# Kernel optimization log

Hardware: AMD Instinct MI355X
Metric: run time of the kernel (lower is better)

## Reference

```python
import jax, jax.numpy as jnp
import numpy as np

SHAPES = ((496, 432), (248, 216), (124, 108))
NS = (40000, 20000, 8000)
T = 32
B = 4
EPS = 1e-3


def _bn(x, g, b, m, v):
    return (x - m) * (g / jnp.sqrt(v + EPS)) + b


def _vfe_scale(voxels, num_pts, w1, p1, w2, p2):
    # voxels: (N, T, 4); num_pts: (N,)
    Tp = voxels.shape[1]
    n = num_pts.astype(voxels.dtype)[:, None, None]
    m3 = voxels[:, :, :3].sum(axis=1, keepdims=True) / n
    m2 = voxels[:, :, :2].sum(axis=1, keepdims=True) / n
    feat = jnp.concatenate([voxels[:, :, :4], voxels[:, :, :3] - m3, voxels[:, :, :2] - m2], axis=-1)  # (N,T,9)
    mask = (jnp.arange(Tp)[None, :] < num_pts[:, None]).astype(voxels.dtype)[:, :, None]
    x = feat
    for w, (g, b_, rm, rv) in ((w1, p1), (w2, p2)):
        h = jax.nn.relu(_bn(jnp.einsum('ntc,cd->ntd', x, w), g, b_, rm, rv))  # (N,T,64)
        gmax = h.max(axis=1, keepdims=True)  # global max includes padded rows, as in torch source
        x = jnp.concatenate([h, jnp.broadcast_to(gmax, h.shape)], axis=-1) * mask  # (N,T,128)
    return x.max(axis=1)[:, :64]  # (N,64)


def _scatter_bev(vf, coords, h, w, batch_size):
    b = coords[:, 0]
    y = jnp.clip(coords[:, 2], 0, h - 1)
    x = jnp.clip(coords[:, 3], 0, w - 1)
    grid = jnp.zeros((batch_size, vf.shape[1], h, w), vf.dtype)
    return grid.at[b, :, y, x].set(vf)


def _fusion(x, w, g, b, m, v):
    y = jax.lax.conv_general_dilated(x, w, (1, 1), ((1, 1), (1, 1)),
                                     dimension_numbers=('NCHW', 'OIHW', 'NCHW'))
    y = _bn(y, g[None, :, None, None], b[None, :, None, None], m[None, :, None, None], v[None, :, None, None])
    return jax.nn.relu(y)


def setup_inputs() -> dict:
    key = jax.random.key(0)
    ks = jax.random.split(key, 32)
    inp = {}
    for s in range(3):
        h, w = SHAPES[s]
        inp[f'voxels_{s}'] = jax.random.normal(ks[s], (NS[s], T, 4), dtype=jnp.float32)
        inp[f'num_pts_{s}'] = jax.random.randint(ks[3 + s], (NS[s],), 1, T + 1, dtype=jnp.int32)
        b = jax.random.randint(ks[6 + s], (NS[s],), 0, B, dtype=jnp.int32)
        z = jnp.zeros((NS[s],), jnp.int32)
        y = jax.random.randint(ks[9 + s], (NS[s],), 0, h, dtype=jnp.int32)
        x = jax.random.randint(ks[12 + s], (NS[s],), 0, w, dtype=jnp.int32)
        inp[f'coords_{s}'] = jnp.stack([b, z, y, x], axis=1)
    # VFE params (stacked across the 3 scales; identical shapes per scale)
    inp['w1'] = jax.random.normal(ks[15], (3, 9, 64), dtype=jnp.float32) * 0.1
    inp['g1'] = jnp.ones((3, 64), jnp.float32) + 0.1 * jax.random.normal(ks[16], (3, 64))
    inp['b1'] = 0.05 * jax.random.normal(ks[17], (3, 64))
    inp['rm1'] = 0.05 * jax.random.normal(ks[18], (3, 64))
    inp['rv1'] = 0.5 + jnp.abs(jax.random.normal(ks[19], (3, 64)))
    inp['w2'] = jax.random.normal(ks[20], (3, 128, 64), dtype=jnp.float32) * 0.05
    inp['g2'] = jnp.ones((3, 64), jnp.float32) + 0.1 * jax.random.normal(ks[21], (3, 64))
    inp['b2'] = 0.05 * jax.random.normal(ks[22], (3, 64))
    inp['rm2'] = 0.05 * jax.random.normal(ks[23], (3, 64))
    inp['rv2'] = 0.5 + jnp.abs(jax.random.normal(ks[24], (3, 64)))
    # Fusion convs (2): Conv2d(128,64,3) + BN
    inp['fw'] = jax.random.normal(ks[25], (2, 64, 128, 3, 3), dtype=jnp.float32) * 0.03
    inp['fg'] = jnp.ones((2, 64), jnp.float32) + 0.1 * jax.random.normal(ks[26], (2, 64))
    inp['fb'] = 0.05 * jax.random.normal(ks[27], (2, 64))
    inp['fm'] = 0.05 * jax.random.normal(ks[28], (2, 64))
    inp['fv'] = 0.5 + jnp.abs(jax.random.normal(ks[29], (2, 64)))
    inp['batch_size'] = B
    return inp


def reference(voxels_0, voxels_1, voxels_2,
              w1, g1, b1, rm1, rv1, w2, g2, b2, rm2, rv2,
              fw, fg, fb, fm, fv,
              num_pts_0, num_pts_1, num_pts_2,
              coords_0, coords_1, coords_2, batch_size):
    voxels = (voxels_0, voxels_1, voxels_2)
    num_pts = (num_pts_0, num_pts_1, num_pts_2)
    coords = (coords_0, coords_1, coords_2)
    sf = []
    for s in range(3):
        vf = _vfe_scale(voxels[s], num_pts[s],
                        w1[s], (g1[s], b1[s], rm1[s], rv1[s]),
                        w2[s], (g2[s], b2[s], rm2[s], rv2[s]))
        h, w = SHAPES[s]
        sf.append(_scatter_bev(vf, coords[s], h, w, batch_size))
    # bottom-up fusion: scale2 -> scale1 -> scale0
    up = jax.image.resize(sf[2], sf[1].shape[:2] + SHAPES[1], method='bilinear')
    fused_1 = _fusion(jnp.concatenate([sf[1], up], axis=1), fw[1], fg[1], fb[1], fm[1], fv[1])
    up = jax.image.resize(fused_1, fused_1.shape[:2] + SHAPES[0], method='bilinear')
    fused_0 = _fusion(jnp.concatenate([sf[0], up], axis=1), fw[0], fg[0], fb[0], fm[0], fv[0])
    return fused_0  # spatial_features_2d: (B, 64, 496, 432)
```

## Files before the change

### kernel.cpp

```cpp
#include <hip/hip_runtime.h>

typedef unsigned short u16;
typedef short bf16x8 __attribute__((ext_vector_type(8)));
typedef float f32x4 __attribute__((ext_vector_type(4)));

#define EPSV 1e-3f

__device__ __forceinline__ float bf2f(u16 u) {
  union { unsigned int i; float f; } x; x.i = ((unsigned int)u) << 16; return x.f;
}
__device__ __forceinline__ u16 f2bf(float f) {
  union { float f; unsigned int i; } x; x.f = f;
  unsigned int r = x.i + 0x7fffu + ((x.i >> 16) & 1u);
  return (u16)(r >> 16);
}

#define WAVE_FENCE() do { __builtin_amdgcn_s_waitcnt(0); __builtin_amdgcn_wave_barrier(); } while (0)

__global__ void twt_kernel(const float* __restrict__ fw, u16* __restrict__ fwT) {
  int i = blockIdx.x * blockDim.x + threadIdx.x;
  if (i >= 2 * 9 * 64 * 128) return;
  int ci = i & 127;
  int r = i >> 7;
  int co = r & 63; r >>= 6;
  int kyx = r % 9;
  int set = r / 9;
  fwT[i] = f2bf(fw[(((set * 64 + co) * 128 + ci) * 9) + kyx]);
}

__global__ __launch_bounds__(256, 2) void vfe_mfma_kernel(
    const float* __restrict__ vox, const int* __restrict__ npts,
    const float* __restrict__ w1, const float* __restrict__ g1, const float* __restrict__ b1,
    const float* __restrict__ rm1, const float* __restrict__ rv1,
    const float* __restrict__ w2, const float* __restrict__ g2, const float* __restrict__ b2,
    const float* __restrict__ rm2, const float* __restrict__ rv2,
    float* __restrict__ vf, int N)
{
  struct PerWave {
    u16 X[32 * 72];
    u16 F[32 * 40];
    u16 G[64];
  };
  __shared__ __align__(16) union {
    struct { u16 W1T[64 * 40]; u16 W2T[64 * 136]; } w;
    PerWave r[4];
  } lds;

  const int tid = threadIdx.x;
  const int lane = tid & 63;
  const int wv = tid >> 6;
  const int m16 = lane & 15;
  const int q = lane >> 4;

  for (int i = tid; i < 64 * 40; i += 256) {
    int c = i / 40, k = i % 40;
    lds.w.W1T[i] = f2bf(k < 9 ? w1[k * 64 + c] : 0.f);
  }
  for (int i = tid; i < 64 * 136; i += 256) {
    int c = i / 136, j = i % 136;
    lds.w.W2T[i] = f2bf(j < 128 ? w2[j * 64 + c] : 0.f);
  }
  __syncthreads();

  bf16x8 bW1[4], bLo[4][2], bHi[4][2];
  float sc1[4], sh1[4], sc2[4], sh2[4];
#pragma unroll
  for (int nf = 0; nf < 4; ++nf) {
    int c = nf * 16 + m16;
    bW1[nf] = *(const bf16x8*)&lds.w.W1T[c * 40 + q * 8];
#pragma unroll
    for (int ks = 0; ks < 2; ++ks) {
      bLo[nf][ks] = *(const bf16x8*)&lds.w.W2T[c * 136 + ks * 32 + q * 8];
      bHi[nf][ks] = *(const bf16x8*)&lds.w.W2T[c * 136 + 64 + ks * 32 + q * 8];
    }
    float s1 = g1[c] * rsqrtf(rv1[c] + EPSV);
    sc1[nf] = s1; sh1[nf] = b1[c] - rm1[c] * s1;
    float s2 = g2[c] * rsqrtf(rv2[c] + EPSV);
    sc2[nf] = s2; sh2[nf] = b2[c] - rm2[c] * s2;
  }
  __syncthreads();

  u16* X = lds.r[wv].X;
  u16* F = lds.r[wv].F;
  u16* G = lds.r[wv].G;
  for (int i = lane; i < 640; i += 64) ((unsigned int*)F)[i] = 0u;

  const int wgid = blockIdx.x * 4 + wv;
  const int wstride = gridDim.x * 4;

  for (int v = wgid; v < N; v += wstride) {
    const int n = npts[v];
    float px = 0.f, py = 0.f, pz = 0.f, pw = 0.f;
    if (lane < 32) {
      float4 u = *(const float4*)(vox + ((size_t)v * 32 + lane) * 4);
      px = u.x; py = u.y; pz = u.z; pw = u.w;
    }
    float sx = px, sy = py, sz = pz;
#pragma unroll
    for (int off = 32; off >= 1; off >>= 1) {
      sx += __shfl_xor(sx, off);
      sy += __shfl_xor(sy, off);
      sz += __shfl_xor(sz, off);
    }
    float nf_ = (float)n;
    float mx = sx / nf_, my = sy / nf_, mz = sz / nf_;
    if (lane < 32) {
      float dx = px - mx, dy = py - my, dz = pz - mz;
      bf16x8 r0, r1;
      r0[0] = (short)f2bf(px); r0[1] = (short)f2bf(py);
      r0[2] = (short)f2bf(pz); r0[3] = (short)f2bf(pw);
      r0[4] = (short)f2bf(dx); r0[5] = (short)f2bf(dy);
      r0[6] = (short)f2bf(dz); r0[7] = (short)f2bf(dx);
      r1 = (bf16x8){0, 0, 0, 0, 0, 0, 0, 0};
      r1[0] = (short)f2bf(dy);
      *(bf16x8*)&F[lane * 40 + 0] = r0;
      *(bf16x8*)&F[lane * 40 + 8] = r1;
    }
    WAVE_FENCE();

    bf16x8 a1[2];
    a1[0] = *(const bf16x8*)&F[m16 * 40 + q * 8];
    a1[1] = *(const bf16x8*)&F[(16 + m16) * 40 + q * 8];
    f32x4 acc1[2][4];
#pragma unroll
    for (int mf = 0; mf < 2; ++mf)
#pragma unroll
      for (int nf = 0; nf < 4; ++nf) {
        acc1[mf][nf] = (f32x4){0.f, 0.f, 0.f, 0.f};
        acc1[mf][nf] = __builtin_amdgcn_mfma_f32_16x16x32_bf16(a1[mf], bW1[nf], acc1[mf][nf], 0, 0, 0);
      }

    float gmx[4] = {0.f, 0.f, 0.f, 0.f};
#pragma unroll
    for (int mf = 0; mf < 2; ++mf)
#pragma unroll
      for (int nf = 0; nf < 4; ++nf)
#pragma unroll
        for (int r = 0; r < 4; ++r) {
          float h = fmaxf(acc1[mf][nf][r] * sc1[nf] + sh1[nf], 0.f);
          gmx[nf] = fmaxf(gmx[nf], h);
          int t = mf * 16 + q * 4 + r;
          X[t * 72 + nf * 16 + m16] = f2bf(h);
        }
#pragma unroll
    for (int nf = 0; nf < 4; ++nf) {
      gmx[nf] = fmaxf(gmx[nf], __shfl_xor(gmx[nf], 16));
      gmx[nf] = fmaxf(gmx[nf], __shfl_xor(gmx[nf], 32));
    }
    if (q == 0) {
#pragma unroll
      for (int nf = 0; nf < 4; ++nf) G[nf * 16 + m16] = f2bf(gmx[nf]);
    }
    WAVE_FENCE();

    f32x4 ga[4];
#pragma unroll
    for (int nf = 0; nf < 4; ++nf) ga[nf] = (f32x4){0.f, 0.f, 0.f, 0.f};
#pragma unroll
    for (int ks = 0; ks < 2; ++ks) {
      bf16x8 ag = (bf16x8){0, 0, 0, 0, 0, 0, 0, 0};
      if (m16 == 0) ag = *(const bf16x8*)&G[ks * 32 + q * 8];
#pragma unroll
      for (int nf = 0; nf < 4; ++nf)
        ga[nf] = __builtin_amdgcn_mfma_f32_16x16x32_bf16(ag, bHi[nf][ks], ga[nf], 0, 0, 0);
    }
    float gt[4];
#pragma unroll
    for (int nf = 0; nf < 4; ++nf) {
      float s = ga[nf][0] + ga[nf][1] + ga[nf][2] + ga[nf][3];
      s += __shfl_xor(s, 16);
      s += __shfl_xor(s, 32);
      gt[nf] = s;
    }

    f32x4 acc2[2][4];
#pragma unroll
    for (int mf = 0; mf < 2; ++mf)
#pragma unroll
      for (int nf = 0; nf < 4; ++nf)
        acc2[mf][nf] = (f32x4){gt[nf], gt[nf], gt[nf], gt[nf]};
#pragma unroll
    for (int ks = 0; ks < 2; ++ks) {
      bf16x8 a2[2];
      a2[0] = *(const bf16x8*)&X[m16 * 72 + ks * 32 + q * 8];
      a2[1] = *(const bf16x8*)&X[(16 + m16) * 72 + ks * 32 + q * 8];
#pragma unroll
      for (int mf = 0; mf < 2; ++mf)
#pragma unroll
        for (int nf = 0; nf < 4; ++nf)
          acc2[mf][nf] = __builtin_amdgcn_mfma_f32_16x16x32_bf16(a2[mf], bLo[nf][ks], acc2[mf][nf], 0, 0, 0);
    }

    float vm[4] = {0.f, 0.f, 0.f, 0.f};
#pragma unroll
    for (int mf = 0; mf < 2; ++mf)
#pragma unroll
      for (int nf = 0; nf < 4; ++nf)
#pragma unroll
        for (int r = 0; r < 4; ++r) {
          int t = mf * 16 + q * 4 + r;
          float h2 = fmaxf(acc2[mf][nf][r] * sc2[nf] + sh2[nf], 0.f);
          if (t < n) vm[nf] = fmaxf(vm[nf], h2);
        }
#pragma unroll
    for (int nf = 0; nf < 4; ++nf) {
      vm[nf] = fmaxf(vm[nf], __shfl_xor(vm[nf], 16));
      vm[nf] = fmaxf(vm[nf], __shfl_xor(vm[nf], 32));
    }
    float outv = (q == 0) ? vm[0] : (q == 1) ? vm[1] : (q == 2) ? vm[2] : vm[3];
    vf[(size_t)v * 64 + q * 16 + m16] = outv;
    __builtin_amdgcn_wave_barrier();
  }
}

__global__ void winner_kernel(const int* __restrict__ coords, int* __restrict__ win,
                              int N, int H, int W) {
  int v = blockIdx.x * blockDim.x + threadIdx.x;
  if (v >= N) return;
  int b = coords[v * 4 + 0];
  int y = min(max(coords[v * 4 + 2], 0), H - 1);
  int x = min(max(coords[v * 4 + 3], 0), W - 1);
  atomicMax(&win[(b * H + y) * W + x], v);
}

__global__ void fill_kernel(const int* __restrict__ win, const float* __restrict__ vf,
                            u16* __restrict__ dst, int cells, int cstride) {
  int i = blockIdx.x * blockDim.x + threadIdx.x;
  if (i >= cells * 8) return;
  int cell = i >> 3, c8 = (i & 7) * 8;
  int wv = win[cell];
  bf16x8 o = (bf16x8){0, 0, 0, 0, 0, 0, 0, 0};
  if (wv >= 0) {
    const float* p = vf + (size_t)wv * 64 + c8;
    float4 v0 = *(const float4*)p;
    float4 v1 = *(const float4*)(p + 4);
    o[0] = (short)f2bf(v0.x); o[1] = (short)f2bf(v0.y);
    o[2] = (short)f2bf(v0.z); o[3] = (short)f2bf(v0.w);
    o[4] = (short)f2bf(v1.x); o[5] = (short)f2bf(v1.y);
    o[6] = (short)f2bf(v1.z); o[7] = (short)f2bf(v1.w);
  }
  *(bf16x8*)&dst[(size_t)cell * cstride + c8] = o;
}

__global__ void upsample_kernel(const u16* __restrict__ src, u16* __restrict__ dst,
                                int Hc, int Wc, int dstride, int doff, int total8) {
  int i = blockIdx.x * blockDim.x + threadIdx.x;
  if (i >= total8) return;
  int c8 = (i & 7) * 8;
  int px = i >> 3;
  int W2 = Wc * 2, H2 = Hc * 2;
  int x = px % W2; int t = px / W2; int y = t % H2; int n = t / H2;
  int ky = y >> 1, kx = x >> 1;
  int ya, yb, xa, xb; float wya, wxa;
  if ((y & 1) == 0) { ya = ky > 0 ? ky - 1 : 0; yb = ky; wya = 0.25f; }
  else              { ya = ky; yb = (ky + 1 < Hc) ? ky + 1 : Hc - 1; wya = 0.75f; }
  if ((x & 1) == 0) { xa = kx > 0 ? kx - 1 : 0; xb = kx; wxa = 0.25f; }
  else              { xa = kx; xb = (kx + 1 < Wc) ? kx + 1 : Wc - 1; wxa = 0.75f; }
  float wyb = 1.f - wya, wxb = 1.f - wxa;
  const u16* sp = src + c8;
  bf16x8 vaa = *(const bf16x8*)&sp[((size_t)(n * Hc + ya) * Wc + xa) * 64];
  bf16x8 vab = *(const bf16x8*)&sp[((size_t)(n * Hc + ya) * Wc + xb) * 64];
  bf16x8 vba = *(const bf16x8*)&sp[((size_t)(n * Hc + yb) * Wc + xa) * 64];
  bf16x8 vbb = *(const bf16x8*)&sp[((size_t)(n * Hc + yb) * Wc + xb) * 64];
  bf16x8 o;
#pragma unroll
  for (int j = 0; j < 8; ++j) {
    float v = wya * (wxa * bf2f((u16)vaa[j]) + wxb * bf2f((u16)vab[j])) +
              wyb * (wxa * bf2f((u16)vba[j]) + wxb * bf2f((u16)vbb[j]));
    o[j] = (short)f2bf(v);
  }
  *(bf16x8*)&dst[(size_t)px * dstride + doff + c8] = o;
}

template<int H, int W, bool NCHW_OUT>
__global__ __launch_bounds__(256, 2) void conv_kernel(
    const u16* __restrict__ in, const u16* __restrict__ wT,
    const float* __restrict__ fg, const float* __restrict__ fb,
    const float* __restrict__ fm, const float* __restrict__ fv,
    void* __restrict__ outv)
{
  constexpr int XT = 32, YT = 16;
  constexpr int XTILES = (W + XT - 1) / XT;
  constexpr int YTILES = (H + YT - 1) / YT;
  constexpr int HC = XT + 2;
  constexpr int NPX = (YT + 2) * HC;
  __shared__ __align__(16) union {
    struct { char A[(NPX / 2) * 128]; char B[9 * 4096]; } s;
    float T[4 * 64 * 33];
  } lds;

  const int tid = threadIdx.x;
  const int lane = tid & 63;
  const int wv = tid >> 6;
  const int m16 = lane & 15;
  const int q = lane >> 4;

  int bid = blockIdx.x;
  const int xt = bid % XTILES; bid /= XTILES;
  const int yt = bid % YTILES;
  const int n = bid / YTILES;
  const int x0 = xt * XT, y0 = yt * YT;

  int lin[8];
#pragma unroll
  for (int mf = 0; mf < 8; ++mf)
    lin[mf] = (wv * 4 + (mf >> 1)) * HC + ((mf & 1) << 4) + m16;

  const int bbase = ((m16 >> 1) << 7) + (((((m16 & 1) << 2) + q) ^ (m16 >> 1)) << 4);

  f32x4 acc[8][4];
#pragma unroll
  for (int mf = 0; mf < 8; ++mf)
#pragma unroll
    for (int nf = 0; nf < 4; ++nf)
      acc[mf][nf] = (f32x4){0.f, 0.f, 0.f, 0.f};

  for (int qk = 0; qk < 4; ++qk) {
    if (qk) __syncthreads();
    {
      const int base_ci = qk * 32;
#pragma unroll
      for (int it = 0; it < 10; ++it) {
        int c = tid + it * 256;
        if (c < NPX * 4) {
          int p = c >> 2, s = c & 3;
          int r = p / HC, xx = p - r * HC;
          int gy = y0 - 1 + r, gx = x0 - 1 + xx;
          uint4 v = make_uint4(0, 0, 0, 0);
          if (gy >= 0 && gy < H && gx >= 0 && gx < W)
            v = *(const uint4*)(in + ((size_t)((n * H + gy) * W + gx)) * 128 + base_ci + s * 8);
          int slot = (((p & 1) << 2) + s) ^ ((p >> 1) & 7);
          *(uint4*)(lds.s.A + ((p >> 1) << 7) + (slot << 4)) = v;
        }
      }
#pragma unroll
      for (int it = 0; it < 9; ++it) {
        int c = tid + it * 256;
        int tap = c >> 8, c2 = c & 255;
        int co = c2 >> 2, s = c2 & 3;
        uint4 v = *(const uint4*)(wT + tap * 8192 + co * 128 + base_ci + s * 8);
        int slot = (((co & 1) << 2) + s) ^ ((co >> 1) & 7);
        *(uint4*)(lds.s.B + (tap << 12) + ((co >> 1) << 7) + (slot << 4)) = v;
      }
    }
    __syncthreads();

#pragma unroll
    for (int tap = 0; tap < 9; ++tap) {
      const int ky = tap / 3, kx = tap - ky * 3;
      const int tapofs = ky * HC + kx;
      bf16x8 b[4];
#pragma unroll
      for (int nf = 0; nf < 4; ++nf)
        b[nf] = *(const bf16x8*)(lds.s.B + (tap << 12) + (nf << 10) + bbase);
      bf16x8 a[8];
#pragma unroll
      for (int mf = 0; mf < 8; ++mf) {
        int hp = lin[mf] + tapofs;
        int slot = (((hp & 1) << 2) + q) ^ ((hp >> 1) & 7);
        a[mf] = *(const bf16x8*)(lds.s.A + ((hp >> 1) << 7) + (slot << 4));
      }
#pragma unroll
      for (int mf = 0; mf < 8; ++mf)
#pragma unroll
        for (int nf = 0; nf < 4; ++nf)
          acc[mf][nf] = __builtin_amdgcn_mfma_f32_16x16x32_bf16(a[mf], b[nf], acc[mf][nf], 0, 0, 0);
    }
  }

  float sc[4], sh[4];
#pragma unroll
  for (int nf = 0; nf < 4; ++nf) {
    int co = nf * 16 + m16;
    float s = fg[co] * rsqrtf(fv[co] + EPSV);
    sc[nf] = s;
    sh[nf] = fb[co] - fm[co] * s;
  }

  if (!NCHW_OUT) {
    u16* out = (u16*)outv;
#pragma unroll
    for (int mf = 0; mf < 8; ++mf) {
      int y = y0 + wv * 4 + (mf >> 1);
      if (y < H) {
#pragma unroll
        for (int nf = 0; nf < 4; ++nf)
#pragma unroll
          for (int r = 0; r < 4; ++r) {
            int px = ((mf & 1) << 4) + q * 4 + r;
            int x = x0 + px;
            if (x < W) {
              int co = nf * 16 + m16;
              float v = fmaxf(acc[mf][nf][r] * sc[nf] + sh[nf], 0.f);
              out[((size_t)(n * H + y) * W + x) * 64 + co] = f2bf(v);
            }
          }
      }
    }
  } else {
    __syncthreads();
    float* out = (float*)outv;
    float* T = &lds.T[wv * 64 * 33];
#pragma unroll
    for (int rr = 0; rr < 4; ++rr) {
      int y = y0 + wv * 4 + rr;
#pragma unroll
      for (int xc = 0; xc < 2; ++xc)
#pragma unroll
        for (int nf = 0; nf < 4; ++nf)
#pragma unroll
          for (int r = 0; r < 4; ++r) {
            int px = (xc << 4) + q * 4 + r;
            int co = nf * 16 + m16;
            T[co * 33 + px] = fmaxf(acc[rr * 2 + xc][nf][r] * sc[nf] + sh[nf], 0.f);
          }
      WAVE_FENCE();
      const int px = lane & 31, co2 = lane >> 5;
      int x = x0 + px;
      if (y < H) {
#pragma unroll 4
        for (int it = 0; it < 32; ++it) {
          int co = it * 2 + co2;
          float v = T[co * 33 + px];
          if (x < W) out[((size_t)(n * 64 + co) * H + y) * W + x] = v;
        }
      }
      WAVE_FENCE();
    }
  }
}

extern "C" void kernel_launch(void* const* d_in, const int* in_sizes, int n_in,
                              void* d_out, int out_size, void* d_ws, size_t ws_size,
                              hipStream_t stream) {
  int I_vox[3], I_np[3], I_co[3];
  int I_w1, I_g1, I_b1, I_rm1, I_rv1, I_w2, I_g2, I_b2, I_rm2, I_rv2;
  int I_fw, I_fg, I_fb, I_fm, I_fv;
  if (in_sizes[1] == 40000) {
    I_vox[0] = 0; I_np[0] = 1; I_co[0] = 2;
    I_vox[1] = 3; I_np[1] = 4; I_co[1] = 5;
    I_vox[2] = 6; I_np[2] = 7; I_co[2] = 8;
    I_w1 = 9; I_g1 = 10; I_b1 = 11; I_rm1 = 12; I_rv1 = 13;
    I_w2 = 14; I_g2 = 15; I_b2 = 16; I_rm2 = 17; I_rv2 = 18;
    I_fw = 19; I_fg = 20; I_fb = 21; I_fm = 22; I_fv = 23;
  } else {
    I_vox[0] = 0; I_vox[1] = 1; I_vox[2] = 2;
    I_w1 = 3; I_g1 = 4; I_b1 = 5; I_rm1 = 6; I_rv1 = 7;
    I_w2 = 8; I_g2 = 9; I_b2 = 10; I_rm2 = 11; I_rv2 = 12;
    I_fw = 13; I_fg = 14; I_fb = 15; I_fm = 16; I_fv = 17;
    I_np[0] = 18; I_np[1] = 19; I_np[2] = 20;
    I_co[0] = 21; I_co[1] = 22; I_co[2] = 23;
  }

  const int HS[3] = {496, 248, 124};
  const int WS[3] = {432, 216, 108};
  int Nv[3];
  for (int s = 0; s < 3; ++s) Nv[s] = in_sizes[I_np[s]];

  char* wsp = (char*)d_ws;
  size_t off = 0;
  auto take = [&](size_t bytes) -> void* {
    void* p = wsp + off;
    off = (off + bytes + 255) & ~(size_t)255;
    return p;
  };
  float* vf[3]; int* win[3];
  for (int s = 0; s < 3; ++s) vf[s] = (float*)take((size_t)Nv[s] * 64 * 4);
  int cells[3];
  for (int s = 0; s < 3; ++s) {
    cells[s] = 4 * HS[s] * WS[s];
    win[s] = (int*)take((size_t)cells[s] * 4);
  }
  u16* buf0 = (u16*)take((size_t)cells[0] * 128 * 2);
  u16* buf1 = (u16*)take((size_t)cells[1] * 128 * 2);
  u16* g2b  = (u16*)take((size_t)cells[2] * 64 * 2);
  u16* fus1 = (u16*)take((size_t)cells[1] * 64 * 2);
  u16* fwT  = (u16*)take((size_t)2 * 9 * 64 * 128 * 2);

  const float* W1 = (const float*)d_in[I_w1];
  const float* G1 = (const float*)d_in[I_g1];
  const float* B1 = (const float*)d_in[I_b1];
  const float* RM1 = (const float*)d_in[I_rm1];
  const float* RV1 = (const float*)d_in[I_rv1];
  const float* W2 = (const float*)d_in[I_w2];
  const float* G2 = (const float*)d_in[I_g2];
  const float* B2 = (const float*)d_in[I_b2];
  const float* RM2 = (const float*)d_in[I_rm2];
  const float* RV2 = (const float*)d_in[I_rv2];
  const float* FW = (const float*)d_in[I_fw];
  const float* FG = (const float*)d_in[I_fg];
  const float* FB = (const float*)d_in[I_fb];
  const float* FM = (const float*)d_in[I_fm];
  const float* FV = (const float*)d_in[I_fv];

  for (int s = 0; s < 3; ++s)
    hipMemsetAsync(win[s], 0xFF, (size_t)cells[s] * 4, stream);

  twt_kernel<<<(2 * 9 * 64 * 128 + 255) / 256, 256, 0, stream>>>(FW, fwT);

  for (int s = 0; s < 3; ++s) {
    int blocks = (Nv[s] + 3) / 4;
    if (blocks > 1024) blocks = 1024;
    vfe_mfma_kernel<<<blocks, 256, 0, stream>>>(
        (const float*)d_in[I_vox[s]], (const int*)d_in[I_np[s]],
        W1 + s * 9 * 64, G1 + s * 64, B1 + s * 64, RM1 + s * 64, RV1 + s * 64,
        W2 + s * 128 * 64, G2 + s * 64, B2 + s * 64, RM2 + s * 64, RV2 + s * 64,
        vf[s], Nv[s]);
  }
  for (int s = 0; s < 3; ++s) {
    winner_kernel<<<(Nv[s] + 255) / 256, 256, 0, stream>>>(
        (const int*)d_in[I_co[s]], win[s], Nv[s], HS[s], WS[s]);
  }
  fill_kernel<<<(cells[0] * 8 + 255) / 256, 256, 0, stream>>>(win[0], vf[0], buf0, cells[0], 128);
  fill_kernel<<<(cells[1] * 8 + 255) / 256, 256, 0, stream>>>(win[1], vf[1], buf1, cells[1], 128);
  fill_kernel<<<(cells[2] * 8 + 255) / 256, 256, 0, stream>>>(win[2], vf[2], g2b, cells[2], 64);

  {
    int total8 = cells[1] * 8;
    upsample_kernel<<<(total8 + 255) / 256, 256, 0, stream>>>(g2b, buf1, 124, 108, 128, 64, total8);
  }
  conv_kernel<248, 216, false><<<4 * ((248 + 15) / 16) * 7, 256, 0, stream>>>(
      buf1, fwT + 9 * 64 * 128, FG + 64, FB + 64, FM + 64, FV + 64, fus1);
  {
    int total8 = cells[0] * 8;
    upsample_kernel<<<(total8 + 255) / 256, 256, 0, stream>>>(fus1, buf0, 248, 216, 128, 64, total8);
  }
  conv_kernel<496, 432, true><<<4 * (496 / 16) * 14, 256, 0, stream>>>(
      buf0, fwT, FG, FB, FM, FV, (float*)d_out);
}
```

Measured before the change: 796.2 us.

## Store conv inputs and weights in channel-quarter planar layout

Reorganizes the 128-channel conv input buffers and the transposed weights into four planes of 32 channels each, so each input-channel-quarter pass of the conv loads a contiguous 64-byte chunk per pixel instead of striding through a 256-byte pixel record. The fill, upsample, weight-transpose and conv kernels are updated consistently. The aim is better cache-line utilization and coalescing for the halo and weight loads. The trade-off is more complex indexing and scattered writes in the fill and upsample kernels.

```diff
diff --git a/kernel.cpp b/kernel.cpp
--- a/kernel.cpp
+++ b/kernel.cpp
@@ -19,13 +19,15 @@
 
 __global__ void twt_kernel(const float* __restrict__ fw, u16* __restrict__ fwT) {
   int i = blockIdx.x * blockDim.x + threadIdx.x;
-  if (i >= 2 * 9 * 64 * 128) return;
-  int ci = i & 127;
-  int r = i >> 7;
+  if (i >= 2 * 4 * 9 * 64 * 32) return;
+  int ciq = i & 31;
+  int r = i >> 5;
   int co = r & 63; r >>= 6;
-  int kyx = r % 9;
-  int set = r / 9;
-  fwT[i] = f2bf(fw[(((set * 64 + co) * 128 + ci) * 9) + kyx]);
+  int tap = r % 9; r /= 9;
+  int qk = r & 3;
+  int set = r >> 2;
+  int ci = qk * 32 + ciq;
+  fwT[i] = f2bf(fw[(((set * 64 + co) * 128 + ci) * 9) + tap]);
 }
 
 __global__ __launch_bounds__(256, 2) void vfe_mfma_kernel(
@@ -224,7 +226,7 @@
 }
 
 __global__ void fill_kernel(const int* __restrict__ win, const float* __restrict__ vf,
-                            u16* __restrict__ dst, int cells, int cstride) {
+                            u16* __restrict__ dst, int cells, size_t ps, int planar) {
   int i = blockIdx.x * blockDim.x + threadIdx.x;
   if (i >= cells * 8) return;
   int cell = i >> 3, c8 = (i & 7) * 8;
@@ -239,11 +241,13 @@
     o[4] = (short)f2bf(v1.x); o[5] = (short)f2bf(v1.y);
     o[6] = (short)f2bf(v1.z); o[7] = (short)f2bf(v1.w);
   }
-  *(bf16x8*)&dst[(size_t)cell * cstride + c8] = o;
+  u16* d = planar ? (dst + (size_t)(c8 >> 5) * ps + (size_t)cell * 32 + (c8 & 31))
+                  : (dst + (size_t)cell * 64 + c8);
+  *(bf16x8*)d = o;
 }
 
 __global__ void upsample_kernel(const u16* __restrict__ src, u16* __restrict__ dst,
-                                int Hc, int Wc, int dstride, int doff, int total8) {
+                                int Hc, int Wc, size_t ps, int total8) {
   int i = blockIdx.x * blockDim.x + threadIdx.x;
   if (i >= total8) return;
   int c8 = (i & 7) * 8;
@@ -269,7 +273,7 @@
               wyb * (wxa * bf2f((u16)vba[j]) + wxb * bf2f((u16)vbb[j]));
     o[j] = (short)f2bf(v);
   }
-  *(bf16x8*)&dst[(size_t)px * dstride + doff + c8] = o;
+  *(bf16x8*)&dst[(size_t)(2 + (c8 >> 5)) * ps + (size_t)px * 32 + (c8 & 31)] = o;
 }
 
 template<int H, int W, bool NCHW_OUT>
@@ -284,6 +288,7 @@
   constexpr int YTILES = (H + YT - 1) / YT;
   constexpr int HC = XT + 2;
   constexpr int NPX = (YT + 2) * HC;
+  const size_t PS = (size_t)4 * H * W * 32;
   __shared__ __align__(16) union {
     struct { char A[(NPX / 2) * 128]; char B[9 * 4096]; } s;
     float T[4 * 64 * 33];
@@ -318,7 +323,7 @@
   for (int qk = 0; qk < 4; ++qk) {
     if (qk) __syncthreads();
     {
-      const int base_ci = qk * 32;
+      const u16* inq = in + (size_t)qk * PS;
 #pragma unroll
       for (int it = 0; it < 10; ++it) {
         int c = tid + it * 256;
@@ -328,17 +333,18 @@
           int gy = y0 - 1 + r, gx = x0 - 1 + xx;
           uint4 v = make_uint4(0, 0, 0, 0);
           if (gy >= 0 && gy < H && gx >= 0 && gx < W)
-            v = *(const uint4*)(in + ((size_t)((n * H + gy) * W + gx)) * 128 + base_ci + s * 8);
+            v = *(const uint4*)(inq + ((size_t)((n * H + gy) * W + gx)) * 32 + s * 8);
           int slot = (((p & 1) << 2) + s) ^ ((p >> 1) & 7);
           *(uint4*)(lds.s.A + ((p >> 1) << 7) + (slot << 4)) = v;
         }
       }
+      const u16* wq = wT + qk * (9 * 64 * 32);
 #pragma unroll
       for (int it = 0; it < 9; ++it) {
         int c = tid + it * 256;
         int tap = c >> 8, c2 = c & 255;
         int co = c2 >> 2, s = c2 & 3;
-        uint4 v = *(const uint4*)(wT + tap * 8192 + co * 128 + base_ci + s * 8);
+        uint4 v = *(const uint4*)(wq + tap * 2048 + co * 32 + s * 8);
         int slot = (((co & 1) << 2) + s) ^ ((co >> 1) & 7);
         *(uint4*)(lds.s.B + (tap << 12) + ((co >> 1) << 7) + (slot << 4)) = v;
       }
@@ -475,7 +481,7 @@
   u16* buf1 = (u16*)take((size_t)cells[1] * 128 * 2);
   u16* g2b  = (u16*)take((size_t)cells[2] * 64 * 2);
   u16* fus1 = (u16*)take((size_t)cells[1] * 64 * 2);
-  u16* fwT  = (u16*)take((size_t)2 * 9 * 64 * 128 * 2);
+  u16* fwT  = (u16*)take((size_t)2 * 4 * 9 * 64 * 32 * 2);
 
   const float* W1 = (const float*)d_in[I_w1];
   const float* G1 = (const float*)d_in[I_g1];
@@ -496,7 +502,7 @@
   for (int s = 0; s < 3; ++s)
     hipMemsetAsync(win[s], 0xFF, (size_t)cells[s] * 4, stream);
 
-  twt_kernel<<<(2 * 9 * 64 * 128 + 255) / 256, 256, 0, stream>>>(FW, fwT);
+  twt_kernel<<<(2 * 4 * 9 * 64 * 32 + 255) / 256, 256, 0, stream>>>(FW, fwT);
 
   for (int s = 0; s < 3; ++s) {
     int blocks = (Nv[s] + 3) / 4;
@@ -511,19 +517,21 @@
     winner_kernel<<<(Nv[s] + 255) / 256, 256, 0, stream>>>(
         (const int*)d_in[I_co[s]], win[s], Nv[s], HS[s], WS[s]);
   }
-  fill_kernel<<<(cells[0] * 8 + 255) / 256, 256, 0, stream>>>(win[0], vf[0], buf0, cells[0], 128);
-  fill_kernel<<<(cells[1] * 8 + 255) / 256, 256, 0, stream>>>(win[1], vf[1], buf1, cells[1], 128);
-  fill_kernel<<<(cells[2] * 8 + 255) / 256, 256, 0, stream>>>(win[2], vf[2], g2b, cells[2], 64);
+  const size_t ps0 = (size_t)cells[0] * 32;
+  const size_t ps1 = (size_t)cells[1] * 32;
+  fill_kernel<<<(cells[0] * 8 + 255) / 256, 256, 0, stream>>>(win[0], vf[0], buf0, cells[0], ps0, 1);
+  fill_kernel<<<(cells[1] * 8 + 255) / 256, 256, 0, stream>>>(win[1], vf[1], buf1, cells[1], ps1, 1);
+  fill_kernel<<<(cells[2] * 8 + 255) / 256, 256, 0, stream>>>(win[2], vf[2], g2b, cells[2], 0, 0);
 
   {
     int total8 = cells[1] * 8;
-    upsample_kernel<<<(total8 + 255) / 256, 256, 0, stream>>>(g2b, buf1, 124, 108, 128, 64, total8);
+    upsample_kernel<<<(total8 + 255) / 256, 256, 0, stream>>>(g2b, buf1, 124, 108, ps1, total8);
   }
   conv_kernel<248, 216, false><<<4 * ((248 + 15) / 16) * 7, 256, 0, stream>>>(
-      buf1, fwT + 9 * 64 * 128, FG + 64, FB + 64, FM + 64, FV + 64, fus1);
+      buf1, fwT + 4 * 9 * 64 * 32, FG + 64, FB + 64, FM + 64, FV + 64, fus1);
   {
     int total8 = cells[0] * 8;
-    upsample_kernel<<<(total8 + 255) / 256, 256, 0, stream>>>(fus1, buf0, 248, 216, 128, 64, total8);
+    upsample_kernel<<<(total8 + 255) / 256, 256, 0, stream>>>(fus1, buf0, 248, 216, ps0, total8);
   }
   conv_kernel<496, 432, true><<<4 * (496 / 16) * 14, 256, 0, stream>>>(
       buf0, fwT, FG, FB, FM, FV, (float*)d_out);
```

Result: faster. 764.3 us (-4.0%).
